# Kernel tuning notes

Hardware: AMD Instinct MI355X
Metric: run time of the kernel (lower is better)

## Reference

```python
import jax, jax.numpy as jnp
import numpy as np

NB_ATOMS = 64
NB_FREE = 8
A = 9                      # atom_size
PAD = (A - 1) // 2         # circular padding for atom convs
TOL = 1e-4
N_ITERS = 20               # fixed-length unroll of the iPALM solver
B, H, W = 4, 1, 128        # y: [B, 1, 128, 128]

DN = ('NCHW', 'OIHW', 'NCHW')


def circ_conv(x, w, pad):
    # F.conv2d(F.pad(x, circular), w)
    xp = jnp.pad(x, ((0, 0), (0, 0), (pad, pad), (pad, pad)), mode='wrap')
    return jax.lax.conv_general_dilated(xp, w, (1, 1), 'VALID', dimension_numbers=DN)


def circ_conv_t(x, w, pad):
    # F.conv2d(pad(x), w.flip(2,3).permute(1,0,2,3))  (adjoint conv, circular)
    wt = jnp.transpose(jnp.flip(w, (2, 3)), (1, 0, 2, 3))
    return circ_conv(x, wt, pad)


def bjorck(Wm, n_iter=15):
    # Bjorck orthonormalization: rows become orthonormal.
    Wm = Wm / jnp.linalg.norm(Wm, ord=2)
    def body(w, _):
        return 1.5 * w - 0.5 * (w @ (w.T @ w)), None
    Wm, _ = jax.lax.scan(body, Wm, None, length=n_iter)
    return Wm


def soft_threshold(x, lmbda):
    # L1 prox
    return jnp.sign(x) * jnp.maximum(jnp.abs(x) - lmbda, 0.0)


def _forward(y, atoms_p, free_atoms_p, beta_p, lmbda):
    dt = y.dtype
    # --- filter preprocessing -------------------------------------------
    fa = bjorck(free_atoms_p.reshape(NB_FREE, -1))                 # [F, A*A]
    gram = fa.T @ fa                                               # [A*A, A*A]
    proj = jnp.eye(A * A, dtype=dt) - gram
    proj_filters = (proj - proj.mean(axis=1)[None, :]).reshape(A * A, 1, A, A)
    dirac = jnp.zeros((1, 1, 2 * A - 1, 2 * A - 1), dt).at[0, 0, A - 1, A - 1].set(1.0)
    proj_impulse = circ_conv_t(circ_conv(dirac, proj_filters, PAD), proj_filters, PAD)  # [1,1,17,17]
    L_pk = jnp.abs(jnp.fft.fft2(proj_impulse, s=(y.shape[2], y.shape[3]))).max()
    beta = jax.nn.relu(beta_p)
    L = 1.01 * beta * L_pk

    atoms = atoms_p - atoms_p.mean(axis=(1, 2, 3), keepdims=True)
    af = atoms.reshape(NB_ATOMS, -1)
    af = af - af @ gram                                            # remove free-atom span
    af = af / jnp.linalg.norm(af, axis=1, keepdims=True)
    af = jnp.sqrt(0.99 / jnp.maximum(beta, 0.1)) * af / jnp.linalg.norm(af, ord=2)
    atoms = af.reshape(NB_ATOMS, 1, A, A)
    Xmat = af @ af.T                                               # [K, K] (1x1 conv)

    # --- iPALM fixed-point iterations -----------------------------------
    coeffs0 = jnp.zeros((y.shape[0], NB_ATOMS, y.shape[2], y.shape[3]), dt)
    active0 = jnp.ones((y.shape[0],), dtype=bool)

    def step(state, k):
        img, new_img, coeffs, new_coeffs, active = state
        m4 = active[:, None, None, None]
        kf = k.astype(dt)
        mom = (kf - 1.0) / (kf + 2.0)

        temp_c = new_coeffs + (new_coeffs - coeffs) * mom
        grad_c = jnp.einsum('oc,bchw->bohw', Xmat, temp_c) - circ_conv(new_img, atoms, PAD)
        upd_c = soft_threshold(temp_c - beta * grad_c, lmbda)
        coeffs2 = jnp.where(m4, new_coeffs, coeffs)
        new_coeffs2 = jnp.where(m4, upd_c, new_coeffs)

        temp_i = new_img + (new_img - img) * mom
        dict_pred = circ_conv_t(new_coeffs2, atoms, PAD)           # [B,1,H,W]
        sum_p = circ_conv(temp_i, proj_impulse, A - 1)             # [B,1,H,W]
        img2 = jnp.where(m4, new_img, img)
        upd_i = temp_i - (temp_i - y + beta * (sum_p - dict_pred)) / L
        new_img2 = jnp.where(m4, upd_i, new_img)

        d = img2 - new_img2
        res = jnp.sqrt(jnp.sum(d * d, axis=(1, 2, 3))) / jnp.sqrt(jnp.sum(img2 * img2, axis=(1, 2, 3)))
        return (img2, new_img2, coeffs2, new_coeffs2, res > TOL), None

    state0 = (y, y, coeffs0, coeffs0, active0)
    (img, new_img, coeffs, new_coeffs, _), _ = jax.lax.scan(
        step, state0, jnp.arange(1, N_ITERS + 1))
    return new_img, new_coeffs


def setup_inputs() -> dict:
    key = jax.random.key(0)
    k1, k2, k3 = jax.random.split(key, 3)
    y = jax.random.normal(k1, (B, H, 128, 128), dtype=jnp.float32)
    atoms = jax.random.normal(k2, (NB_ATOMS, 1, A, A), dtype=jnp.float32) / 3000.0
    free_atoms = jax.random.normal(k3, (NB_FREE, 1, A, A), dtype=jnp.float32) / 3000.0
    beta = jnp.asarray(1.0, dtype=jnp.float32)
    lmbda = jnp.asarray(1e-3, dtype=jnp.float32)
    return {"y": y, "atoms": atoms, "free_atoms": free_atoms, "beta": beta, "lmbda": lmbda}


def reference(y, atoms, free_atoms, beta, lmbda):
    return _forward(y, atoms, free_atoms, beta, lmbda)
```

## Files before the change

kernel.cpp:

```cpp
#include <hip/hip_runtime.h>
#include <math.h>


#define NB 4
#define NCH 64
#define NPIX 16384
#define NPB (NCH*NPIX)
#define NCOEF (NB*NCH*NPIX)
#define NIMG  (NB*NPIX)
#define NPG 32
#define TOLV 1e-4f

#define SC_BETA 0
#define SC_L    1
#define SC_G    4
#define SC_G2   5
#define SC_LPK2 6

__global__ __launch_bounds__(256) void k_prep1(const float* __restrict__ fatoms,
    const float* __restrict__ beta_p,
    float* __restrict__ gram_g, float* __restrict__ pf_g,
    float* __restrict__ scalars)
{
    __shared__ float sW[648], sWf[648];
    __shared__ float sG[64], sP[64], sF[64], sT[64], sTmp[64];
    __shared__ float sGr[6561];
    __shared__ float rs[81];
    __shared__ float sSig;
    int tid = threadIdx.x;
    if (tid==0){ float b=beta_p[0]; scalars[SC_BETA]=(b>0.f)?b:0.f;
                 ((unsigned*)scalars)[SC_LPK2]=0u; }
    for (int e=tid; e<648; e+=256) sW[e]=fatoms[e];
    __syncthreads();
    if (tid<64){ int r=tid>>3, s=tid&7; float a=0.f;
        for (int k=0;k<81;++k) a=fmaf(sW[r*81+k],sW[s*81+k],a); sG[tid]=a; }
    __syncthreads();
    if (tid<64){
        int r8 = tid&7;
        float v = 1.f;
        for (int it=0; it<64; ++it){
            float nv=0.f;
            #pragma unroll
            for (int j=0;j<8;++j) nv = fmaf(sG[r8*8+j], __shfl(v,j,8), nv);
            float m = fabsf(nv);
            m = fmaxf(m, __shfl_xor(m,1,8));
            m = fmaxf(m, __shfl_xor(m,2,8));
            m = fmaxf(m, __shfl_xor(m,4,8));
            v = nv/m;
        }
        float wv=0.f;
        #pragma unroll
        for (int j=0;j<8;++j) wv = fmaf(sG[r8*8+j], __shfl(v,j,8), wv);
        float num=v*wv, den=v*v;
        num += __shfl_xor(num,1,8); num += __shfl_xor(num,2,8); num += __shfl_xor(num,4,8);
        den += __shfl_xor(den,1,8); den += __shfl_xor(den,2,8); den += __shfl_xor(den,4,8);
        if (tid==0) sSig = sqrtf(num/den);
    }
    __syncthreads();
    float inv_s = 1.f/sSig;
    for (int e=tid; e<648; e+=256) sW[e]*=inv_s;
    if (tid<64){ sG[tid]*=inv_s*inv_s; sP[tid]=((tid>>3)==(tid&7))?1.f:0.f; }
    __syncthreads();
    for (int it=0; it<15; ++it){
        if (tid<64) sF[tid] = (((tid>>3)==(tid&7))?1.5f:0.f) - 0.5f*sG[tid];
        __syncthreads();
        if (tid<64){ int r=tid>>3, c=tid&7; float ap=0.f, ag=0.f;
            #pragma unroll
            for (int k=0;k<8;++k){ float f=sF[r*8+k]; ap=fmaf(f,sP[k*8+c],ap); ag=fmaf(f,sG[k*8+c],ag); }
            sTmp[tid]=ap; sT[tid]=ag; }
        __syncthreads();
        if (tid<64){ int r=tid>>3, c=tid&7; float g2=0.f;
            #pragma unroll
            for (int k=0;k<8;++k) g2=fmaf(sT[r*8+k],sF[k*8+c],g2);
            sG[tid]=g2; sP[tid]=sTmp[tid]; }
        __syncthreads();
    }
    for (int e=tid; e<648; e+=256){ int r=e/81, j=e%81; float a=0.f;
        #pragma unroll
        for (int k=0;k<8;++k) a=fmaf(sP[r*8+k], sW[k*81+j], a);
        sWf[e]=a; }
    __syncthreads();
    for (int e=tid; e<6561; e+=256){ int i=e/81, j=e%81; float a=0.f;
        #pragma unroll
        for (int r=0;r<8;++r) a=fmaf(sWf[r*81+i],sWf[r*81+j],a);
        sGr[e]=a; gram_g[e]=a; }
    __syncthreads();
    if (tid<81){ float s=0.f; for (int k=0;k<81;++k) s+=sGr[tid*81+k]; rs[tid]=(1.f-s)/81.f; }
    __syncthreads();
    for (int e=tid; e<6561; e+=256){ int i=e/81, j=e%81;
        pf_g[e] = ((i==j)?1.f:0.f) - sGr[e] - rs[j]; }
}

__global__ __launch_bounds__(256) void k_PP(const float* __restrict__ pf, float* __restrict__ PP)
{
    __shared__ float spf[6561];
    for (int e=threadIdx.x; e<6561; e+=256) spf[e]=pf[e];
    __syncthreads();
    int e = blockIdx.x*256 + threadIdx.x;
    if (e>=6561) return;
    int al=e/81, be=e%81; float a=0.f;
    for (int c=0;c<81;++c) a=fmaf(spf[c*81+al], spf[c*81+be], a);
    PP[e]=a;
}

__global__ void k_impulse(const float* __restrict__ PP, float* __restrict__ pi)
{
    int t = threadIdx.x;
    if (t>=289) return;
    int h=t/17, w=t%17;
    float acc=0.f;
    for (int p=0;p<9;++p){
        int i2=(h+p-4+17)%17;
        if (i2<4||i2>12) continue;
        for (int q=0;q<9;++q){
            int j2=(w+q-4+17)%17;
            if (j2<4||j2>12) continue;
            int al=(12-i2)*9+(12-j2);
            int be=(8-p)*9+(8-q);
            acc += PP[al*81+be];
        }
    }
    pi[t]=acc;
}

__global__ __launch_bounds__(64) void k_dft(const float* __restrict__ pi, float* __restrict__ scalars)
{
    __shared__ float spi[289], ct[128], st[128];
    int tid=threadIdx.x; int gid=blockIdx.x*64+tid;
    for (int e=tid; e<289; e+=64) spi[e]=pi[e];
    for (int e=tid; e<128; e+=64){ float ang=(float)e*(6.28318530717958647692f/128.f);
                  ct[e]=cosf(ang); st[e]=sinf(ang); }
    __syncthreads();
    int u=gid>>7, v=gid&127;
    float re=0.f, im=0.f;
    for (int i=0;i<17;++i){
        int ku=(u*i)&127;
        const float* prow=spi+i*17;
        for (int j=0;j<17;++j){
            int k=(ku+v*j)&127;
            float x=prow[j];
            re=fmaf(x,ct[k],re); im=fmaf(x,st[k],im);
        }
    }
    float m2=re*re+im*im;
    #pragma unroll
    for (int d=32; d; d>>=1) m2=fmaxf(m2, __shfl_down(m2,d));
    if (tid==0) atomicMax(((unsigned*)scalars)+SC_LPK2, __float_as_uint(m2));
}

__global__ __launch_bounds__(128) void k_atoms1(const float* __restrict__ atoms_in,
    const float* __restrict__ gram, float* __restrict__ af_rn, float* __restrict__ af_rnT)
{
    int a=blockIdx.x, tid=threadIdx.x;
    __shared__ float a0[81], a1[81], rbuf[128];
    float v = (tid<81)? atoms_in[a*81+tid] : 0.f;
    rbuf[tid]=v; __syncthreads();
    for (int off=64; off; off>>=1){ if (tid<off) rbuf[tid]+=rbuf[tid+off]; __syncthreads(); }
    float mean = rbuf[0]/81.f;
    __syncthreads();
    if (tid<81) a0[tid]=v-mean;
    __syncthreads();
    float w=0.f;
    if (tid<81){ float dot=0.f;
        for (int k=0;k<81;++k) dot=fmaf(a0[k], gram[k*81+tid], dot);
        w=a0[tid]-dot; a1[tid]=w; }
    rbuf[tid]=(tid<81)? w*w : 0.f;
    __syncthreads();
    for (int off=64; off; off>>=1){ if (tid<off) rbuf[tid]+=rbuf[tid+off]; __syncthreads(); }
    float inv = 1.f/sqrtf(rbuf[0]);
    if (tid<81){ float r=a1[tid]*inv; af_rn[a*81+tid]=r; af_rnT[tid*64+a]=r; }
}

__global__ __launch_bounds__(256) void k_M(const float* __restrict__ af_rn,
    const float* __restrict__ af_rnT, float* __restrict__ M)
{
    int e=blockIdx.x*256+threadIdx.x;
    int i=e>>6, j=e&63;
    float a=0.f;
    for (int k=0;k<81;++k) a=fmaf(af_rn[i*81+k], af_rnT[(k<<6)+j], a);
    M[e]=a;
}

__global__ __launch_bounds__(256) void k_M2(const float* __restrict__ IN,
    float* __restrict__ OUT)
{
    int e=blockIdx.x*256+threadIdx.x;
    int i=e>>6, j=e&63;
    float a=0.f;
    for (int k=0;k<64;++k) a=fmaf(IN[(i<<6)+k], IN[(k<<6)+j], a);
    OUT[e]=a;
}

__global__ __launch_bounds__(256) void k_fin(const float* __restrict__ Mg,
    const float* __restrict__ MPg, const float* __restrict__ af_rn,
    float* __restrict__ scalars,
    float* __restrict__ atoms_f, float* __restrict__ atomsT, float* __restrict__ Xmat)
{
    __shared__ float sM[4096];
    __shared__ float sGc[2];
    int tid=threadIdx.x;
    for (int e=tid; e<4096; e+=256) sM[e]=Mg[e];
    __syncthreads();
    if (tid<64){
        float m[64];
        const float4* mp = reinterpret_cast<const float4*>(MPg + (tid<<6));
        #pragma unroll
        for (int j4=0;j4<16;++j4){
            float4 v4=mp[j4];
            m[j4*4+0]=v4.x; m[j4*4+1]=v4.y; m[j4*4+2]=v4.z; m[j4*4+3]=v4.w;
        }
        float v = 1.0f + 0.01f*(float)tid;
        for (int it=0; it<8; ++it){
            float a0=0.f,a1=0.f,a2=0.f,a3=0.f;
            #pragma unroll
            for (int j=0;j<64;j+=4){
                a0=fmaf(m[j+0], __shfl(v,j+0), a0);
                a1=fmaf(m[j+1], __shfl(v,j+1), a1);
                a2=fmaf(m[j+2], __shfl(v,j+2), a2);
                a3=fmaf(m[j+3], __shfl(v,j+3), a3);
            }
            float nv=(a0+a1)+(a2+a3);
            float mx=fabsf(nv);
            #pragma unroll
            for (int d=1; d<64; d<<=1) mx=fmaxf(mx, __shfl_xor(mx,d));
            v=nv/mx;
        }
        float w0=0.f,w1=0.f,w2=0.f,w3=0.f;
        #pragma unroll
        for (int j=0;j<64;j+=4){
            w0=fmaf(sM[(tid<<6)+j+0], __shfl(v,j+0), w0);
            w1=fmaf(sM[(tid<<6)+j+1], __shfl(v,j+1), w1);
            w2=fmaf(sM[(tid<<6)+j+2], __shfl(v,j+2), w2);
            w3=fmaf(sM[(tid<<6)+j+3], __shfl(v,j+3), w3);
        }
        float wv=(w0+w1)+(w2+w3);
        float num=v*wv, den=v*v;
        #pragma unroll
        for (int d=1; d<64; d<<=1){ num+=__shfl_xor(num,d); den+=__shfl_xor(den,d); }
        if (tid==0){
            float sig = sqrtf(num/den);
            float b = scalars[SC_BETA];
            float s = sqrtf(0.99f/fmaxf(b,0.1f));
            float g = s/sig;
            scalars[SC_G]=g; scalars[SC_G2]=g*g;
            float lpk = sqrtf(__uint_as_float(((unsigned*)scalars)[SC_LPK2]));
            scalars[SC_L] = 1.01f*b*lpk;
            sGc[0]=g; sGc[1]=g*g;
        }
    }
    __syncthreads();
    float g=sGc[0], g2=sGc[1];
    for (int idx=tid; idx<5184; idx+=256){
        int a=idx/81, pq=idx-a*81;
        float v=g*af_rn[idx];
        atoms_f[idx]=v;
        atomsT[pq*64+a]=v;
    }
    for (int e=tid; e<4096; e+=256) Xmat[e]=g2*sM[e];
}

template<bool FIRST>
__global__ __launch_bounds__(512,4) void kA(const float* __restrict__ c_in,
    const float* __restrict__ nc_in, const float* __restrict__ nimg,
    const float* __restrict__ Xmat, const float* __restrict__ atomsT,
    const float* __restrict__ scalars, const float* __restrict__ lmbda_p,
    const float* __restrict__ red_in,
    float* __restrict__ c_out, float* __restrict__ nc_out, float mom)
{
    int b=blockIdx.y, h0=blockIdx.x;
    int tid=threadIdx.x;
    int wv = __builtin_amdgcn_readfirstlane(tid>>6);
    int lane = tid&63;
    int co = wv*8;
    int px = lane*2;
    __shared__ float sTemp[64*128];
    __shared__ float simg[9*128];
    __shared__ float sAct;
    if (FIRST){ if (tid==0) sAct=1.f; }
    else if (tid<64){
        float sd=red_in[(b<<7)+(tid<<1)], si=red_in[(b<<7)+(tid<<1)+1];
        #pragma unroll
        for (int off=32; off; off>>=1){ sd+=__shfl_down(sd,off); si+=__shfl_down(si,off); }
        if (tid==0) sAct = (sd > TOLV*TOLV*si) ? 1.f : 0.f;
    }
    for (int e=tid; e<1152; e+=512)
        simg[e]=nimg[b*NPIX + (((h0-4+(e>>7))&127)<<7) + (e&127)];
    size_t sbase = (size_t)b*NPB + (h0<<7);
    float2 nv8[8], cv8[8];
    if (!FIRST){
        #pragma unroll
        for (int oc=0;oc<8;++oc){
            size_t a = sbase + (size_t)(co+oc)*NPIX + px;
            cv8[oc]=*reinterpret_cast<const float2*>(c_in + a);
            nv8[oc]=*reinterpret_cast<const float2*>(nc_in + a);
            float2 t;
            t.x=fmaf(mom,nv8[oc].x-cv8[oc].x,nv8[oc].x);
            t.y=fmaf(mom,nv8[oc].y-cv8[oc].y,nv8[oc].y);
            *reinterpret_cast<float2*>(sTemp + (co+oc)*128 + px) = t;
        }
    }
    __syncthreads();
    const float* Xo = Xmat + co;
    const float* Ao = atomsT + co;
    float acc[16];
    #pragma unroll
    for (int i=0;i<16;++i) acc[i]=0.f;
    if (!FIRST){
        for (int c=0;c<64;++c){
            float2 t=*reinterpret_cast<const float2*>(sTemp + c*128 + px);
            const float* Xr = Xo + (c<<6);
            #pragma unroll
            for (int oc=0;oc<8;++oc){
                float x=Xr[oc];
                acc[oc*2+0]=fmaf(x,t.x,acc[oc*2+0]);
                acc[oc*2+1]=fmaf(x,t.y,acc[oc*2+1]);
            }
        }
    }
    for (int p=0;p<9;++p){
        const float* srow = simg + p*128;
        float in10[10];
        #pragma unroll
        for (int j=0;j<10;++j) in10[j]=srow[(px-4+j)&127];
        #pragma unroll 3
        for (int q=0;q<9;++q){
            const float* Ar = Ao + ((p*9+q)<<6);
            #pragma unroll
            for (int oc=0;oc<8;++oc){
                float a=Ar[oc];
                acc[oc*2+0]=fmaf(a,-in10[q+0],acc[oc*2+0]);
                acc[oc*2+1]=fmaf(a,-in10[q+1],acc[oc*2+1]);
            }
        }
    }
    float beta=scalars[SC_BETA], lmb=lmbda_p[0];
    bool act = (sAct!=0.f);
    #pragma unroll
    for (int oc=0;oc<8;++oc){
        size_t a = sbase + (size_t)(co+oc)*NPIX + px;
        float2 nv, cv;
        if (FIRST){ nv=make_float2(0.f,0.f); cv=nv; }
        else { nv=nv8[oc]; cv=cv8[oc]; }
        float2 nw, cw;
        {
            float t=FIRST?0.f:fmaf(mom,nv.x-cv.x,nv.x);
            float u=fmaf(-beta,acc[oc*2+0],t); float au=fabsf(u)-lmb;
            u=(au>0.f)?copysignf(au,u):0.f; nw.x=act?u:nv.x; cw.x=act?nv.x:cv.x;
        }{
            float t=FIRST?0.f:fmaf(mom,nv.y-cv.y,nv.y);
            float u=fmaf(-beta,acc[oc*2+1],t); float au=fabsf(u)-lmb;
            u=(au>0.f)?copysignf(au,u):0.f; nw.y=act?u:nv.y; cw.y=act?nv.y:cv.y;
        }
        *reinterpret_cast<float2*>(c_out  + a) = cw;
        *reinterpret_cast<float2*>(nc_out + a) = nw;
    }
}

__global__ __launch_bounds__(256,4) void kB1(const float* __restrict__ nc2,
    const float* __restrict__ atoms_f, float* __restrict__ part)
{
    int b=blockIdx.z, cg=blockIdx.y, pb=blockIdx.x;
    int t=threadIdx.x;
    int row = pb*16 + (t>>4);
    int cb  = (t&15)*8;
    const float* src = nc2 + (b*NCH + cg*2)*NPIX;
    float acc[8];
    #pragma unroll
    for (int k=0;k<8;++k) acc[k]=0.f;
    for (int c=0;c<2;++c){
        const float* chan = src + c*NPIX;
        const float* arow = atoms_f + (cg*2+c)*81;
        #pragma unroll 3
        for (int p=0;p<9;++p){
            int r=(row+4-p)&127;
            const float* rp_ = chan + (r<<7);
            float in16[16];
            #pragma unroll
            for (int k4=0;k4<4;++k4){
                int col=(cb-4+(k4<<2))&127;
                const float4 vv = *reinterpret_cast<const float4*>(rp_+col);
                in16[(k4<<2)+0]=vv.x; in16[(k4<<2)+1]=vv.y;
                in16[(k4<<2)+2]=vv.z; in16[(k4<<2)+3]=vv.w;
            }
            #pragma unroll
            for (int q=0;q<9;++q){
                float a = arow[p*9+q];
                #pragma unroll
                for (int k=0;k<8;++k) acc[k]=fmaf(in16[k+8-q], a, acc[k]);
            }
        }
    }
    float* dst = part + (cg*NB+b)*NPIX + (row<<7) + cb;
    #pragma unroll
    for (int k=0;k<8;++k) dst[k]=acc[k];
}

template<bool FIRST>
__global__ __launch_bounds__(512) void kB2(const float* __restrict__ img,
    const float* __restrict__ nimg, const float* __restrict__ y,
    const float* __restrict__ part, const float* __restrict__ pi,
    const float* __restrict__ scalars, const float* __restrict__ red_in,
    float* __restrict__ img_out, float* __restrict__ nimg_out,
    float* __restrict__ red_out, float mom)
{
    int b=blockIdx.y, rp=blockIdx.x;
    int tid=threadIdx.x;
    int half=tid>>8, lid=tid&255;
    int ty=lid>>7, w=lid&127;
    int h0=rp*2;
    __shared__ float sti[18*128];
    __shared__ float spi[289];
    __shared__ float sP2[256];
    __shared__ float rsd[4], rsi[4];
    __shared__ float sAct;
    if (FIRST){ if (tid==0) sAct=1.f; }
    else if (tid<64){
        float sd=red_in[(b<<7)+(tid<<1)], si=red_in[(b<<7)+(tid<<1)+1];
        #pragma unroll
        for (int off=32; off; off>>=1){ sd+=__shfl_down(sd,off); si+=__shfl_down(si,off); }
        if (tid==0) sAct = (sd > TOLV*TOLV*si) ? 1.f : 0.f;
    }
    const float* ib  = img  + b*NPIX;
    const float* nib = nimg + b*NPIX;
    for (int e=tid; e<2304; e+=512){
        int r=e>>7, cc=e&127;
        int idx=(((h0-8+r)&127)<<7)+cc;
        float nv=nib[idx], v=ib[idx];
        sti[e]=fmaf(mom, nv-v, nv);
    }
    for (int e=tid; e<289; e+=512) spi[e]=pi[e];
    __syncthreads();
    float sp=0.f;
    int pn = 9 - half;
    for (int pk=0; pk<pn; ++pk){
        int p = half*9 + pk;
        const float* srow = sti + (ty+p)*128;
        const float* pr = spi + p*17;
        #pragma unroll
        for (int q=0;q<17;++q) sp=fmaf(srow[(w+q-8)&127], pr[q], sp);
    }
    if (half==1) sP2[lid]=sp;
    __syncthreads();
    if (tid<256){
        sp += sP2[lid];
        int pix=((h0+ty)<<7)+w;
        float dp=0.f;
        #pragma unroll
        for (int g=0; g<NPG; ++g) dp += part[(g*NB+b)*NPIX + pix];
        float ti = sti[(ty+8)*128 + w];
        float beta=scalars[SC_BETA], L=scalars[SC_L];
        float yv=y[b*NPIX+pix];
        float upd = ti - (ti - yv + beta*(sp - dp))/L;
        bool act = (sAct!=0.f);
        float iv=ib[pix], niv=nib[pix];
        float i2 = act? niv : iv;
        float ni2 = act? upd : niv;
        img_out[b*NPIX+pix]=i2;
        nimg_out[b*NPIX+pix]=ni2;
        float d=i2-ni2;
        float sd=d*d, si=i2*i2;
        #pragma unroll
        for (int off=32; off; off>>=1){ sd+=__shfl_down(sd,off); si+=__shfl_down(si,off); }
        if ((tid&63)==0){ rsd[tid>>6]=sd; rsi[tid>>6]=si; }
    }
    __syncthreads();
    if (tid==0){
        float a=rsd[0]+rsd[1]+rsd[2]+rsd[3];
        float c2=rsi[0]+rsi[1]+rsi[2]+rsi[3];
        red_out[(b<<7)+(rp<<1)+0]=a;
        red_out[(b<<7)+(rp<<1)+1]=c2;
    }
}

extern "C" void kernel_launch(void* const* d_in, const int* in_sizes, int n_in,
                              void* d_out, int out_size, void* d_ws, size_t ws_size,
                              hipStream_t stream)
{
    const float* y        = (const float*)d_in[0];
    const float* atoms_p  = (const float*)d_in[1];
    const float* fatoms_p = (const float*)d_in[2];
    const float* beta_p   = (const float*)d_in[3];
    const float* lmbda_p  = (const float*)d_in[4];
    float* out = (float*)d_out;
    float* w = (float*)d_ws;

    size_t off=0;
    float* cb[2];  cb[0]=w+off;  off+=NCOEF; cb[1]=w+off;  off+=NCOEF;
    float* ncb[2]; ncb[0]=w+off; off+=NCOEF; ncb[1]=w+off; off+=NCOEF;
    float* ib[2];  ib[0]=w+off;  off+=NIMG;  ib[1]=w+off;  off+=NIMG;
    float* nib[2]; nib[0]=w+off; off+=NIMG;  nib[1]=w+off; off+=NIMG;
    float* part=w+off;    off+=NPG*NIMG;
    float* red[2]; red[0]=w+off; off+=512; red[1]=w+off; off+=512;
    float* gram=w+off;    off+=6561;
    float* pf=w+off;      off+=6561;
    float* PP=w+off;      off+=6561;
    float* pi=w+off;      off+=512;
    float* af_rn=w+off;   off+=5184;
    float* af_rnT=w+off;  off+=5184;
    float* Mmat=w+off;    off+=4096;
    float* MA=w+off;      off+=4096;
    float* MB=w+off;      off+=4096;
    float* atoms_f=w+off; off+=5184;
    float* atomsT=w+off;  off+=5184;
    float* Xmat=w+off;    off+=4096;
    float* scalars=w+off; off+=32;

    k_prep1<<<dim3(1),dim3(256),0,stream>>>(fatoms_p, beta_p, gram, pf, scalars);
    k_PP<<<dim3(26),dim3(256),0,stream>>>(pf, PP);
    k_impulse<<<dim3(1),dim3(320),0,stream>>>(PP, pi);
    k_dft<<<dim3(256),dim3(64),0,stream>>>(pi, scalars);
    k_atoms1<<<dim3(64),dim3(128),0,stream>>>(atoms_p, gram, af_rn, af_rnT);
    k_M<<<dim3(16),dim3(256),0,stream>>>(af_rn, af_rnT, Mmat);
    k_M2<<<dim3(16),dim3(256),0,stream>>>(Mmat, MA);
    k_M2<<<dim3(16),dim3(256),0,stream>>>(MA, MB);
    k_M2<<<dim3(16),dim3(256),0,stream>>>(MB, MA);
    k_M2<<<dim3(16),dim3(256),0,stream>>>(MA, MB);
    k_fin<<<dim3(1),dim3(256),0,stream>>>(Mmat, MB, af_rn, scalars, atoms_f, atomsT, Xmat);

    int p=0;
    for (int k=1; k<=20; ++k){
        float mom = (float)(k-1)/(float)(k+2);
        const float* rin = red[(k-1)&1];
        float* rout = red[k&1];
        const float* img_i  = (k==1)? y : ib[p];
        const float* nimg_i = (k==1)? y : nib[p];
        float* nc_t  = (k==20)? (out+NIMG) : ncb[p^1];
        float* nimg_t= (k==20)? out : nib[p^1];
        if (k==1){
            kA<true><<<dim3(128,4),dim3(512),0,stream>>>(cb[p],ncb[p],nimg_i,Xmat,atomsT,
                scalars,lmbda_p,rin, cb[p^1],nc_t,mom);
        } else {
            kA<false><<<dim3(128,4),dim3(512),0,stream>>>(cb[p],ncb[p],nimg_i,Xmat,atomsT,
                scalars,lmbda_p,rin, cb[p^1],nc_t,mom);
        }
        kB1<<<dim3(8,32,4),dim3(256),0,stream>>>(nc_t, atoms_f, part);
        if (k==1){
            kB2<true><<<dim3(64,4),dim3(512),0,stream>>>(img_i,nimg_i,y,part,pi,scalars,rin,
                ib[p^1],nimg_t,rout,mom);
        } else {
            kB2<false><<<dim3(64,4),dim3(512),0,stream>>>(img_i,nimg_i,y,part,pi,scalars,rin,
                ib[p^1],nimg_t,rout,mom);
        }
        p^=1;
    }
}
```

Before: 1.188 ms.

## Rotate three coefficient buffers to drop the per-iteration previous-coefficient write

Replaces the double-buffered coeffs/new_coeffs pairs with a three-buffer rotation, so the 'previous coefficients' of the next iteration are simply the current new_coeffs buffer and need not be copied out. kA now writes only the new coefficients, plus a write back into the input buffer when the batch is inactive, or zeros on the first iteration. This removes roughly one full 16 MB coefficient write per iteration. The cost is more complex aliasing logic: kA now writes into a buffer declared __restrict__ that it also reads, and the inactive-batch case relies on the rotation order being correct.

```diff
diff --git a/kernel.cpp b/kernel.cpp
--- a/kernel.cpp
+++ b/kernel.cpp
@@ -261,11 +261,11 @@
 
 template<bool FIRST>
 __global__ __launch_bounds__(512,4) void kA(const float* __restrict__ c_in,
-    const float* __restrict__ nc_in, const float* __restrict__ nimg,
+    float* __restrict__ nc_in, const float* __restrict__ nimg,
     const float* __restrict__ Xmat, const float* __restrict__ atomsT,
     const float* __restrict__ scalars, const float* __restrict__ lmbda_p,
     const float* __restrict__ red_in,
-    float* __restrict__ c_out, float* __restrict__ nc_out, float mom)
+    float* __restrict__ nc_out, float mom)
 {
     int b=blockIdx.y, h0=blockIdx.x;
     int tid=threadIdx.x;
@@ -341,18 +341,22 @@
         float2 nv, cv;
         if (FIRST){ nv=make_float2(0.f,0.f); cv=nv; }
         else { nv=nv8[oc]; cv=cv8[oc]; }
-        float2 nw, cw;
+        float2 nw;
         {
             float t=FIRST?0.f:fmaf(mom,nv.x-cv.x,nv.x);
             float u=fmaf(-beta,acc[oc*2+0],t); float au=fabsf(u)-lmb;
-            u=(au>0.f)?copysignf(au,u):0.f; nw.x=act?u:nv.x; cw.x=act?nv.x:cv.x;
+            u=(au>0.f)?copysignf(au,u):0.f; nw.x=act?u:nv.x;
         }{
             float t=FIRST?0.f:fmaf(mom,nv.y-cv.y,nv.y);
             float u=fmaf(-beta,acc[oc*2+1],t); float au=fabsf(u)-lmb;
-            u=(au>0.f)?copysignf(au,u):0.f; nw.y=act?u:nv.y; cw.y=act?nv.y:cv.y;
-        }
-        *reinterpret_cast<float2*>(c_out  + a) = cw;
+            u=(au>0.f)?copysignf(au,u):0.f; nw.y=act?u:nv.y;
+        }
         *reinterpret_cast<float2*>(nc_out + a) = nw;
+        if (FIRST){
+            *reinterpret_cast<float2*>(nc_in + a) = make_float2(0.f,0.f);
+        } else if (!act){
+            *reinterpret_cast<float2*>(nc_in + a) = cv;
+        }
     }
 }
 
@@ -485,8 +489,7 @@
     float* w = (float*)d_ws;
 
     size_t off=0;
-    float* cb[2];  cb[0]=w+off;  off+=NCOEF; cb[1]=w+off;  off+=NCOEF;
-    float* ncb[2]; ncb[0]=w+off; off+=NCOEF; ncb[1]=w+off; off+=NCOEF;
+    float* cf[3];  cf[0]=w+off; off+=NCOEF; cf[1]=w+off; off+=NCOEF; cf[2]=w+off; off+=NCOEF;
     float* ib[2];  ib[0]=w+off;  off+=NIMG;  ib[1]=w+off;  off+=NIMG;
     float* nib[2]; nib[0]=w+off; off+=NIMG;  nib[1]=w+off; off+=NIMG;
     float* part=w+off;    off+=NPG*NIMG;
@@ -517,6 +520,7 @@
     k_M2<<<dim3(16),dim3(256),0,stream>>>(MA, MB);
     k_fin<<<dim3(1),dim3(256),0,stream>>>(Mmat, MB, af_rn, scalars, atoms_f, atomsT, Xmat);
 
+    int ic=0, in=1, io=2;
     int p=0;
     for (int k=1; k<=20; ++k){
         float mom = (float)(k-1)/(float)(k+2);
@@ -524,14 +528,14 @@
         float* rout = red[k&1];
         const float* img_i  = (k==1)? y : ib[p];
         const float* nimg_i = (k==1)? y : nib[p];
-        float* nc_t  = (k==20)? (out+NIMG) : ncb[p^1];
+        float* nc_t  = (k==20)? (out+NIMG) : cf[io];
         float* nimg_t= (k==20)? out : nib[p^1];
         if (k==1){
-            kA<true><<<dim3(128,4),dim3(512),0,stream>>>(cb[p],ncb[p],nimg_i,Xmat,atomsT,
-                scalars,lmbda_p,rin, cb[p^1],nc_t,mom);
+            kA<true><<<dim3(128,4),dim3(512),0,stream>>>(cf[ic],cf[in],nimg_i,Xmat,atomsT,
+                scalars,lmbda_p,rin, nc_t,mom);
         } else {
-            kA<false><<<dim3(128,4),dim3(512),0,stream>>>(cb[p],ncb[p],nimg_i,Xmat,atomsT,
-                scalars,lmbda_p,rin, cb[p^1],nc_t,mom);
+            kA<false><<<dim3(128,4),dim3(512),0,stream>>>(cf[ic],cf[in],nimg_i,Xmat,atomsT,
+                scalars,lmbda_p,rin, nc_t,mom);
         }
         kB1<<<dim3(8,32,4),dim3(256),0,stream>>>(nc_t, atoms_f, part);
         if (k==1){
@@ -541,6 +545,7 @@
             kB2<false><<<dim3(64,4),dim3(512),0,stream>>>(img_i,nimg_i,y,part,pi,scalars,rin,
                 ib[p^1],nimg_t,rout,mom);
         }
+        int t=ic; ic=in; in=io; io=t;
         p^=1;
     }
 }
```

Result: faster. 1.160 ms (median of 2 runs) (-2.4%).
